# Kernel tuning notes

Measured on AMD Instinct MI355X. Metric: run time of the kernel, lower is better.

## Reference

```python
import jax, jax.numpy as jnp
import numpy as np

B, C, H, W = 4, 512, 64, 64
CK = C // 8  # key/query channels


def setup_inputs() -> dict:
    key = jax.random.key(0)
    ks = jax.random.split(key, 4)
    x = jax.random.normal(ks[0], (B, C, H, W), dtype=jnp.float32)
    # 1x1 conv weights -> plain [out, in] matrices; fan-in scaled like torch default-ish
    Wf = jax.random.normal(ks[1], (CK, C), dtype=jnp.float32) * (1.0 / np.sqrt(C))
    Wg = jax.random.normal(ks[2], (CK, C), dtype=jnp.float32) * (1.0 / np.sqrt(C))
    Wh = jax.random.normal(ks[3], (C, C), dtype=jnp.float32) * (1.0 / np.sqrt(C))
    bf = jnp.zeros((CK,), dtype=jnp.float32)
    bg = jnp.zeros((CK,), dtype=jnp.float32)
    bh = jnp.zeros((C,), dtype=jnp.float32)
    gamma = jnp.zeros((1,), dtype=jnp.float32)
    return {"x": x, "Wf": Wf, "bf": bf, "Wg": Wg, "bg": bg, "Wh": Wh, "bh": bh, "gamma": gamma}


def reference(x, Wf, bf, Wg, bg, Wh, bh, gamma):
    b, c, h, w = x.shape
    n = h * w
    xf = x.reshape(b, c, n)  # [B, C, N]
    # 1x1 convs == per-pixel linear maps
    f = jnp.einsum('kc,bcn->bkn', Wf, xf) + bf[None, :, None]  # [B, CK, N]
    g = jnp.einsum('kc,bcn->bkn', Wg, xf) + bg[None, :, None]  # [B, CK, N]
    hx = jnp.einsum('oc,bcn->bon', Wh, xf) + bh[None, :, None]  # [B, C, N]
    # energy[b,i,j] = sum_k f[b,k,i] * g[b,k,j]  (f_x.permute(0,2,1) @ g_x)
    energy = jnp.einsum('bki,bkj->bij', f, g)  # [B, N, N]
    attention = jax.nn.softmax(energy, axis=-1)
    # out[b,c,i] = sum_j hx[b,c,j] * attention[b,i,j]  (h_x @ attention^T)
    out = jnp.einsum('bcj,bij->bci', hx, attention)  # [B, C, N]
    out = out.reshape(b, c, h, w)
    return gamma[0] * out + x
```

## Files before the change

### kernel.cpp

```cpp
#include <hip/hip_runtime.h>
#include <hip/hip_bf16.h>

#define NB 4
#define CC 512
#define NN 4096
#define CKK 64

typedef _Float16 f16x8 __attribute__((ext_vector_type(8)));
typedef float    f32x4 __attribute__((ext_vector_type(4)));

__device__ __forceinline__ void g2l16(const _Float16* g, _Float16* l) {
    __builtin_amdgcn_global_load_lds(
        (const __attribute__((address_space(1))) void*)g,
        (__attribute__((address_space(3))) void*)l, 16, 0, 0);
}

__device__ __forceinline__ void stage_tile(const _Float16* __restrict__ g, int ldg,
                                           _Float16* lds, int lane, int wave) {
    #pragma unroll
    for (int r = 0; r < 2; r++) {
        int q = r * 4 + wave;
        int row = q * 16 + (lane >> 2);
        int col = (lane & 3) * 8;
        g2l16(g + (size_t)row * ldg + col, lds + q * 512 + lane * 8);
    }
}

__device__ __forceinline__ void stage_swz(const _Float16* __restrict__ g, int ldg,
                                          _Float16* lds, int tid) {
    int row = tid >> 2;
    int scq = (tid & 3) ^ ((row >> 1) & 3);
    g2l16(g + (size_t)row * ldg + scq * 8, lds + tid * 8);
}

__device__ __forceinline__ f16x8 rd_swz(const _Float16* lds, int row, int quad) {
    int q = quad ^ ((row >> 1) & 3);
    return *(const f16x8*)(lds + row * 32 + q * 8);
}

__launch_bounds__(256)
__global__ void prep(const float* __restrict__ x, _Float16* __restrict__ xT,
                     const float* __restrict__ Wf, const float* __restrict__ bf_,
                     const float* __restrict__ Wg, const float* __restrict__ bg_,
                     const float* __restrict__ Wh, const float* __restrict__ bh_,
                     _Float16* __restrict__ Wall, float* __restrict__ Ball) {
    const int N = NN, C = CC;
    int bid = blockIdx.x;
    int t = threadIdx.x;
    if (bid < 2048) {
        int n0 = (bid & 63) << 6;
        int c0 = ((bid >> 6) & 7) << 6;
        int b  = bid >> 9;
        __shared__ float T[64][65];
        const float* xb = x + (size_t)b * C * N;
        #pragma unroll
        for (int r = 0; r < 4; r++) {
            int c = (t >> 4) + 16 * r;
            int n4 = (t & 15) * 4;
            float4 v = *(const float4*)(xb + (size_t)(c0 + c) * N + n0 + n4);
            T[n4 + 0][c] = v.x; T[n4 + 1][c] = v.y; T[n4 + 2][c] = v.z; T[n4 + 3][c] = v.w;
        }
        __syncthreads();
        int n = t >> 2, cb = (t & 3) * 16;
        f16x8 h0, h1;
        #pragma unroll
        for (int i = 0; i < 8; i++) { h0[i] = (_Float16)T[n][cb + i]; h1[i] = (_Float16)T[n][cb + 8 + i]; }
        _Float16* dst = xT + (size_t)b * N * C + (size_t)(n0 + n) * C + c0 + cb;
        *(f16x8*)dst = h0;
        *(f16x8*)(dst + 8) = h1;
    } else {
        int o = bid - 2048;
        const float* src;
        if (o < 64)       src = Wf + (size_t)o * C;
        else if (o < 128) src = Wg + (size_t)(o - 64) * C;
        else              src = Wh + (size_t)(o - 128) * C;
        Wall[(size_t)o * C + t]       = (_Float16)src[t];
        Wall[(size_t)o * C + 256 + t] = (_Float16)src[256 + t];
        if (t == 0)
            Ball[o] = (o < 64) ? bf_[o] : (o < 128 ? bg_[o - 64] : bh_[o - 128]);
    }
}

__launch_bounds__(256)
__global__ void proj_mfma(const _Float16* __restrict__ xT, const _Float16* __restrict__ Wall,
                          const float* __restrict__ Ball,
                          _Float16* __restrict__ Ft, _Float16* __restrict__ Gt,
                          _Float16* __restrict__ Hx) {
    const int N = NN, C = CC;
    int n0 = blockIdx.x * 128;
    int o0 = blockIdx.y * 128;
    int b  = blockIdx.z;
    const _Float16* Arow = Wall + (size_t)o0 * C;
    const _Float16* Brow = xT + (size_t)b * N * C + (size_t)n0 * C;
    __shared__ _Float16 As[128 * 32];
    __shared__ _Float16 Bs[128 * 32];
    int tid = threadIdx.x, lane = tid & 63, wave = tid >> 6;
    int wm = wave & 1, wn = wave >> 1, lrow = lane & 15, quad = lane >> 4;
    f32x4 acc[4][4] = {};
    for (int kc = 0; kc < C; kc += 32) {
        __syncthreads();
        stage_tile(Arow + kc, C, As, lane, wave);
        stage_tile(Brow + kc, C, Bs, lane, wave);
        __syncthreads();
        f16x8 af[4], bf[4];
        #pragma unroll
        for (int mi = 0; mi < 4; mi++)
            af[mi] = *(const f16x8*)(As + (wm * 64 + mi * 16 + lrow) * 32 + quad * 8);
        #pragma unroll
        for (int ni = 0; ni < 4; ni++)
            bf[ni] = *(const f16x8*)(Bs + (wn * 64 + ni * 16 + lrow) * 32 + quad * 8);
        #pragma unroll
        for (int mi = 0; mi < 4; mi++)
            #pragma unroll
            for (int ni = 0; ni < 4; ni++)
                acc[mi][ni] = __builtin_amdgcn_mfma_f32_16x16x32_f16(af[mi], bf[ni], acc[mi][ni], 0, 0, 0);
    }
    float bias_r[4][4];
    #pragma unroll
    for (int mi = 0; mi < 4; mi++)
        #pragma unroll
        for (int r = 0; r < 4; r++)
            bias_r[mi][r] = Ball[o0 + wm * 64 + mi * 16 + quad * 4 + r];
    _Float16* Ftb = Ft + (size_t)b * NN * CKK;
    _Float16* Gtb = Gt + (size_t)b * NN * CKK;
    _Float16* Hxb = Hx + (size_t)b * CC * N;
    #pragma unroll
    for (int mi = 0; mi < 4; mi++)
        #pragma unroll
        for (int ni = 0; ni < 4; ni++)
            #pragma unroll
            for (int r = 0; r < 4; r++) {
                int o = o0 + wm * 64 + mi * 16 + quad * 4 + r;
                int n = n0 + wn * 64 + ni * 16 + lrow;
                _Float16 v = (_Float16)(acc[mi][ni][r] + bias_r[mi][r]);
                if (o < 64)       Ftb[(size_t)n * CKK + o] = v;
                else if (o < 128) Gtb[(size_t)n * CKK + (o - 64)] = v;
                else              Hxb[(size_t)(o - 128) * N + n] = v;
            }
}

#define PST_LD  136
#define MRED_LD 34
#define SM_FT    0
#define SM_BSG   16384
#define SM_PST   32768
#define SM_AH    67584
#define SM_MRED  100352
#define SM_MRUN  117760
#define SM_LRUN  118272
#define SM_OSC   118784
#define SM_TOTAL 119296

__launch_bounds__(512, 2)
__global__ void attn_fused(const _Float16* __restrict__ Ft, const _Float16* __restrict__ Gt,
                           const _Float16* __restrict__ Hx, const float* __restrict__ x,
                           const float* __restrict__ gamma, float* __restrict__ out) {
    const int N = NN, C = CC;
    extern __shared__ char smem[];
    _Float16* FtL = (_Float16*)(smem + SM_FT);
    _Float16* BsG = (_Float16*)(smem + SM_BSG);
    _Float16* Pst = (_Float16*)(smem + SM_PST);
    _Float16* Ah  = (_Float16*)(smem + SM_AH);
    float* Mred = (float*)(smem + SM_MRED);
    float* Mrun = (float*)(smem + SM_MRUN);
    float* Lrun = (float*)(smem + SM_LRUN);
    float* Osc  = (float*)(smem + SM_OSC);

    const int b  = blockIdx.z;
    const int i0 = blockIdx.x * 128;
    const int c0 = blockIdx.y * 256;
    const int tid = threadIdx.x;
    const int lane = tid & 63, w = tid >> 6;
    const int lrow = lane & 15, quad = lane >> 4;
    const int wi = w & 3, wj = w >> 2;
    const int wc = w >> 1, wi2 = w & 1;

    const _Float16* Ftb = Ft + (size_t)b * N * CKK + (size_t)i0 * CKK;
    const _Float16* Gtb = Gt + (size_t)b * N * CKK;
    const _Float16* Hxb = Hx + (size_t)b * C * N + (size_t)c0 * N;

    stage_swz(Ftb,      CKK, FtL,        tid);
    stage_swz(Ftb + 32, CKK, FtL + 4096, tid);
    if (tid < 128) { Mrun[tid] = -1e30f; Lrun[tid] = 0.0f; }
    __syncthreads();

    f16x8 afs[2][2];
    #pragma unroll
    for (int mi = 0; mi < 2; mi++)
        #pragma unroll
        for (int ks = 0; ks < 2; ks++)
            afs[mi][ks] = rd_swz(FtL + ks * 4096, wi * 32 + mi * 16 + lrow, quad);

    f32x4 acc[4][4] = {};

    for (int jt = 0; jt < NN / 128; jt++) {
        const _Float16* Gtr = Gtb + (size_t)jt * 128 * CKK;
        stage_swz(Gtr,      CKK, BsG,        tid);
        stage_swz(Gtr + 32, CKK, BsG + 4096, tid);
        __syncthreads();

        f32x4 sacc[2][4] = {};
        #pragma unroll
        for (int ks = 0; ks < 2; ks++)
            #pragma unroll
            for (int ni = 0; ni < 4; ni++) {
                f16x8 bfs = rd_swz(BsG + ks * 4096, wj * 64 + ni * 16 + lrow, quad);
                #pragma unroll
                for (int mi = 0; mi < 2; mi++)
                    sacc[mi][ni] = __builtin_amdgcn_mfma_f32_16x16x32_f16(afs[mi][ks], bfs, sacc[mi][ni], 0, 0, 0);
            }
        #pragma unroll
        for (int mi = 0; mi < 2; mi++)
            #pragma unroll
            for (int r = 0; r < 4; r++) {
                float v = fmaxf(fmaxf(sacc[mi][0][r], sacc[mi][1][r]),
                                fmaxf(sacc[mi][2][r], sacc[mi][3][r]));
                int row = wi * 32 + mi * 16 + quad * 4 + r;
                Mred[row * MRED_LD + wj * 16 + lrow] = v;
            }
        __syncthreads();
        if (tid < 128) {
            const float* mr = Mred + tid * MRED_LD;
            float mt = mr[0];
            #pragma unroll
            for (int k = 1; k < 32; k++) mt = fmaxf(mt, mr[k]);
            float mo = Mrun[tid];
            float mn = fmaxf(mo, mt);
            float sc = __expf(mo - mn);
            Mrun[tid] = mn;
            Osc[tid] = sc;
            Lrun[tid] *= sc;
        }
        __syncthreads();
        #pragma unroll
        for (int mi = 0; mi < 2; mi++)
            #pragma unroll
            for (int r = 0; r < 4; r++) {
                int row = wi * 32 + mi * 16 + quad * 4 + r;
                float m = Mrun[row];
                float ls = 0.f;
                #pragma unroll
                for (int ni = 0; ni < 4; ni++) {
                    float s16 = (float)(_Float16)sacc[mi][ni][r];
                    _Float16 p16 = (_Float16)__expf(s16 - m);
                    Pst[row * PST_LD + wj * 64 + ni * 16 + lrow] = p16;
                    ls += (float)p16;
                }
                Mred[row * MRED_LD + wj * 16 + lrow] = ls;
            }
        float scv[4];
        #pragma unroll
        for (int ni = 0; ni < 4; ni++) scv[ni] = Osc[wi2 * 64 + ni * 16 + lrow];
        #pragma unroll
        for (int mi = 0; mi < 4; mi++)
            #pragma unroll
            for (int ni = 0; ni < 4; ni++)
                #pragma unroll
                for (int r = 0; r < 4; r++)
                    acc[mi][ni][r] *= scv[ni];
        __syncthreads();
        if (tid < 128) {
            const float* mr = Mred + tid * MRED_LD;
            float s = 0.f;
            #pragma unroll
            for (int k = 0; k < 32; k++) s += mr[k];
            Lrun[tid] += s;
        }
        const _Float16* Hxr = Hxb + (size_t)jt * 128;
        stage_swz(Hxr,                   N, Ah,        tid);
        stage_swz(Hxr + (size_t)128 * N, N, Ah + 4096, tid);
        #pragma unroll
        for (int kk = 0; kk < 4; kk++) {
            if (kk < 3) {
                const _Float16* src = Hxr + (kk + 1) * 32;
                _Float16* dst = Ah + ((kk + 1) & 1) * 8192;
                stage_swz(src,                   N, dst,        tid);
                stage_swz(src + (size_t)128 * N, N, dst + 4096, tid);
            }
            __syncthreads();
            const _Float16* A = Ah + (kk & 1) * 8192;
            f16x8 bfv[4];
            #pragma unroll
            for (int ni = 0; ni < 4; ni++)
                bfv[ni] = *(const f16x8*)(Pst + (wi2 * 64 + ni * 16 + lrow) * PST_LD + kk * 32 + quad * 8);
            #pragma unroll
            for (int mi = 0; mi < 4; mi++) {
                f16x8 av = rd_swz(A, wc * 64 + mi * 16 + lrow, quad);
                #pragma unroll
                for (int ni = 0; ni < 4; ni++)
                    acc[mi][ni] = __builtin_amdgcn_mfma_f32_16x16x32_f16(av, bfv[ni], acc[mi][ni], 0, 0, 0);
            }
        }
    }
    __syncthreads();
    if (tid < 128) Osc[tid] = 1.0f / Lrun[tid];
    __syncthreads();
    float gv = gamma[0];
    const float* xb = x + (size_t)b * C * N;
    float* ob = out + (size_t)b * C * N;
    float li[4];
    #pragma unroll
    for (int ni = 0; ni < 4; ni++) li[ni] = Osc[wi2 * 64 + ni * 16 + lrow];
    #pragma unroll
    for (int mi = 0; mi < 4; mi++)
        #pragma unroll
        for (int ni = 0; ni < 4; ni++)
            #pragma unroll
            for (int r = 0; r < 4; r++) {
                int c = c0 + wc * 64 + mi * 16 + quad * 4 + r;
                int i = i0 + wi2 * 64 + ni * 16 + lrow;
                ob[(size_t)c * N + i] = gv * (acc[mi][ni][r] * li[ni]) + xb[(size_t)c * N + i];
            }
}

extern "C" void kernel_launch(void* const* d_in, const int* in_sizes, int n_in,
                              void* d_out, int out_size, void* d_ws, size_t ws_size,
                              hipStream_t stream) {
    const float* x     = (const float*)d_in[0];
    const float* Wf    = (const float*)d_in[1];
    const float* bf    = (const float*)d_in[2];
    const float* Wg    = (const float*)d_in[3];
    const float* bg    = (const float*)d_in[4];
    const float* Wh    = (const float*)d_in[5];
    const float* bh    = (const float*)d_in[6];
    const float* gamma = (const float*)d_in[7];
    float* out = (float*)d_out;

    char* wsb = (char*)d_ws;
    _Float16* Wall = (_Float16*)wsb;
    float*    Ball = (float*)(wsb + ((size_t)768 << 10));
    _Float16* Ft = (_Float16*)(wsb + ((size_t)1 << 20));
    _Float16* Gt = (_Float16*)(wsb + ((size_t)3 << 20));
    _Float16* Hx = (_Float16*)(wsb + ((size_t)5 << 20));
    _Float16* xT = (_Float16*)(wsb + ((size_t)21 << 20));

    prep<<<dim3(2048 + 640), dim3(256), 0, stream>>>(
        x, xT, Wf, bf, Wg, bg, Wh, bh, Wall, Ball);
    proj_mfma<<<dim3(NN / 128, 5, NB), dim3(256), 0, stream>>>(xT, Wall, Ball, Ft, Gt, Hx);

    hipFuncSetAttribute((const void*)attn_fused,
                        hipFuncAttributeMaxDynamicSharedMemorySize, SM_TOTAL);
    attn_fused<<<dim3(NN / 128, CC / 256, NB), dim3(512), SM_TOTAL, stream>>>(
        Ft, Gt, Hx, x, gamma, out);
}
```

Before: 275.3 us.

## Pipeline G and Hx tile loads with vmcnt barriers and shuffle-based softmax reductions

New measurement: 292.0 us. 6.1% more time.

```diff
diff --git a/kernel.cpp b/kernel.cpp
--- a/kernel.cpp
+++ b/kernel.cpp
@@ -5,9 +5,15 @@
 #define CC 512
 #define NN 4096
 #define CKK 64
-
+#define NT 32
+
+typedef _Float16 f16x4 __attribute__((ext_vector_type(4)));
 typedef _Float16 f16x8 __attribute__((ext_vector_type(8)));
 typedef float    f32x4 __attribute__((ext_vector_type(4)));
+
+#define BAR()       asm volatile("s_barrier" ::: "memory")
+#define BAR_LGKM()  asm volatile("s_waitcnt lgkmcnt(0)\n\ts_barrier" ::: "memory")
+#define BAR_VM(n)   asm volatile("s_waitcnt vmcnt(" #n ")\n\ts_barrier" ::: "memory")
 
 __device__ __forceinline__ void g2l16(const _Float16* g, _Float16* l) {
     __builtin_amdgcn_global_load_lds(
@@ -127,44 +133,50 @@
     #pragma unroll
     for (int mi = 0; mi < 4; mi++)
         #pragma unroll
-        for (int ni = 0; ni < 4; ni++)
-            #pragma unroll
-            for (int r = 0; r < 4; r++) {
-                int o = o0 + wm * 64 + mi * 16 + quad * 4 + r;
-                int n = n0 + wn * 64 + ni * 16 + lrow;
-                _Float16 v = (_Float16)(acc[mi][ni][r] + bias_r[mi][r]);
-                if (o < 64)       Ftb[(size_t)n * CKK + o] = v;
-                else if (o < 128) Gtb[(size_t)n * CKK + (o - 64)] = v;
-                else              Hxb[(size_t)(o - 128) * N + n] = v;
-            }
+        for (int ni = 0; ni < 4; ni++) {
+            int o = o0 + wm * 64 + mi * 16 + quad * 4;
+            int n = n0 + wn * 64 + ni * 16 + lrow;
+            f16x4 v;
+            #pragma unroll
+            for (int r = 0; r < 4; r++) v[r] = (_Float16)(acc[mi][ni][r] + bias_r[mi][r]);
+            if (o < 64)       *(f16x4*)(Ftb + (size_t)n * CKK + o) = v;
+            else if (o < 128) *(f16x4*)(Gtb + (size_t)n * CKK + (o - 64)) = v;
+            else {
+                #pragma unroll
+                for (int r = 0; r < 4; r++)
+                    Hxb[(size_t)(o - 128 + r) * N + n] = v[r];
+            }
+        }
 }
 
 #define PST_LD  136
-#define MRED_LD 34
+#define MRL     9
 #define SM_FT    0
 #define SM_BSG   16384
-#define SM_PST   32768
-#define SM_AH    67584
-#define SM_MRED  100352
-#define SM_MRUN  117760
-#define SM_LRUN  118272
-#define SM_OSC   118784
-#define SM_TOTAL 119296
+#define SM_PST   49152
+#define SM_AH    83968
+#define SM_MRED  149504
+#define SM_MRUN  154112
+#define SM_LRUN  154624
+#define SM_OSC   155136
+#define SM_FLAG  155648
+#define SM_TOTAL 155776
 
 __launch_bounds__(512, 2)
 __global__ void attn_fused(const _Float16* __restrict__ Ft, const _Float16* __restrict__ Gt,
                            const _Float16* __restrict__ Hx, const float* __restrict__ x,
                            const float* __restrict__ gamma, float* __restrict__ out) {
-    const int N = NN, C = CC;
+    const int N = NN;
     extern __shared__ char smem[];
-    _Float16* FtL = (_Float16*)(smem + SM_FT);
-    _Float16* BsG = (_Float16*)(smem + SM_BSG);
-    _Float16* Pst = (_Float16*)(smem + SM_PST);
-    _Float16* Ah  = (_Float16*)(smem + SM_AH);
+    _Float16* FtL  = (_Float16*)(smem + SM_FT);
+    _Float16* BsGp = (_Float16*)(smem + SM_BSG);
+    _Float16* Pst  = (_Float16*)(smem + SM_PST);
+    _Float16* AhL  = (_Float16*)(smem + SM_AH);
     float* Mred = (float*)(smem + SM_MRED);
     float* Mrun = (float*)(smem + SM_MRUN);
     float* Lrun = (float*)(smem + SM_LRUN);
     float* Osc  = (float*)(smem + SM_OSC);
+    int*   Fl   = (int*)(smem + SM_FLAG);
 
     const int b  = blockIdx.z;
     const int i0 = blockIdx.x * 128;
@@ -177,11 +189,14 @@
 
     const _Float16* Ftb = Ft + (size_t)b * N * CKK + (size_t)i0 * CKK;
     const _Float16* Gtb = Gt + (size_t)b * N * CKK;
-    const _Float16* Hxb = Hx + (size_t)b * C * N + (size_t)c0 * N;
+    const _Float16* Hxb = Hx + (size_t)b * CC * N + (size_t)c0 * N;
 
     stage_swz(Ftb,      CKK, FtL,        tid);
     stage_swz(Ftb + 32, CKK, FtL + 4096, tid);
+    stage_swz(Gtb,      CKK, BsGp,        tid);
+    stage_swz(Gtb + 32, CKK, BsGp + 4096, tid);
     if (tid < 128) { Mrun[tid] = -1e30f; Lrun[tid] = 0.0f; }
+    if (tid == 0) Fl[0] = 0;
     __syncthreads();
 
     f16x8 afs[2][2];
@@ -193,45 +208,74 @@
 
     f32x4 acc[4][4] = {};
 
-    for (int jt = 0; jt < NN / 128; jt++) {
-        const _Float16* Gtr = Gtb + (size_t)jt * 128 * CKK;
-        stage_swz(Gtr,      CKK, BsG,        tid);
-        stage_swz(Gtr + 32, CKK, BsG + 4096, tid);
-        __syncthreads();
-
+    #pragma unroll 1
+    for (int jt = 0; jt < NT; jt++) {
+        const int cur = jt & 1;
+        const _Float16* Hxr = Hxb + (size_t)jt * 128;
+        stage_swz(Hxr,                        N, AhL,         tid);
+        stage_swz(Hxr + (size_t)128 * N,      N, AhL + 4096,  tid);
+        stage_swz(Hxr + 32,                   N, AhL + 8192,  tid);
+        stage_swz(Hxr + 32 + (size_t)128 * N, N, AhL + 12288, tid);
+        stage_swz(Hxr + 64,                   N, AhL + 16384, tid);
+        stage_swz(Hxr + 64 + (size_t)128 * N, N, AhL + 20480, tid);
+        stage_swz(Hxr + 96,                   N, AhL + 24576, tid);
+        stage_swz(Hxr + 96 + (size_t)128 * N, N, AhL + 28672, tid);
+        const _Float16* Gn = Gtb + (size_t)((jt + 1) & (NT - 1)) * 128 * CKK;
+        _Float16* Gdst = BsGp + (cur ^ 1) * 8192;
+        stage_swz(Gn,      CKK, Gdst,        tid);
+        stage_swz(Gn + 32, CKK, Gdst + 4096, tid);
+        BAR_VM(10);
+
+        const _Float16* Bst = BsGp + cur * 8192;
         f32x4 sacc[2][4] = {};
         #pragma unroll
         for (int ks = 0; ks < 2; ks++)
             #pragma unroll
             for (int ni = 0; ni < 4; ni++) {
-                f16x8 bfs = rd_swz(BsG + ks * 4096, wj * 64 + ni * 16 + lrow, quad);
+                f16x8 bfs = rd_swz(Bst + ks * 4096, wj * 64 + ni * 16 + lrow, quad);
                 #pragma unroll
                 for (int mi = 0; mi < 2; mi++)
                     sacc[mi][ni] = __builtin_amdgcn_mfma_f32_16x16x32_f16(afs[mi][ks], bfs, sacc[mi][ni], 0, 0, 0);
             }
+        float red[8];
         #pragma unroll
         for (int mi = 0; mi < 2; mi++)
             #pragma unroll
-            for (int r = 0; r < 4; r++) {
-                float v = fmaxf(fmaxf(sacc[mi][0][r], sacc[mi][1][r]),
-                                fmaxf(sacc[mi][2][r], sacc[mi][3][r]));
-                int row = wi * 32 + mi * 16 + quad * 4 + r;
-                Mred[row * MRED_LD + wj * 16 + lrow] = v;
-            }
-        __syncthreads();
+            for (int r = 0; r < 4; r++)
+                red[mi * 4 + r] = fmaxf(fmaxf(sacc[mi][0][r], sacc[mi][1][r]),
+                                        fmaxf(sacc[mi][2][r], sacc[mi][3][r]));
+        #pragma unroll
+        for (int off = 1; off < 8; off <<= 1)
+            #pragma unroll
+            for (int s = 0; s < 8; s++)
+                red[s] = fmaxf(red[s], __shfl_xor(red[s], off));
+        if ((lrow & 7) == 0) {
+            #pragma unroll
+            for (int mi = 0; mi < 2; mi++)
+                #pragma unroll
+                for (int r = 0; r < 4; r++)
+                    Mred[(wi * 32 + mi * 16 + quad * 4 + r) * MRL + wj * 2 + (lrow >> 3)] = red[mi * 4 + r];
+        }
+        BAR_LGKM();
+
         if (tid < 128) {
-            const float* mr = Mred + tid * MRED_LD;
+            const float* mr = Mred + tid * MRL;
             float mt = mr[0];
             #pragma unroll
-            for (int k = 1; k < 32; k++) mt = fmaxf(mt, mr[k]);
+            for (int k = 1; k < 8; k++) mt = fmaxf(mt, mr[k]);
             float mo = Mrun[tid];
-            float mn = fmaxf(mo, mt);
-            float sc = __expf(mo - mn);
-            Mrun[tid] = mn;
-            Osc[tid] = sc;
-            Lrun[tid] *= sc;
-        }
-        __syncthreads();
+            if (mt > mo) {
+                Fl[0] = 1;
+                Mrun[tid] = mt;
+                float sc = __expf(mo - mt);
+                Osc[tid] = sc;
+                Lrun[tid] *= sc;
+            } else {
+                Osc[tid] = 1.0f;
+            }
+        }
+        BAR_LGKM();
+
         #pragma unroll
         for (int mi = 0; mi < 2; mi++)
             #pragma unroll
@@ -241,63 +285,77 @@
                 float ls = 0.f;
                 #pragma unroll
                 for (int ni = 0; ni < 4; ni++) {
-                    float s16 = (float)(_Float16)sacc[mi][ni][r];
-                    _Float16 p16 = (_Float16)__expf(s16 - m);
+                    _Float16 p16 = (_Float16)__expf(sacc[mi][ni][r] - m);
                     Pst[row * PST_LD + wj * 64 + ni * 16 + lrow] = p16;
                     ls += (float)p16;
                 }
-                Mred[row * MRED_LD + wj * 16 + lrow] = ls;
-            }
-        float scv[4];
-        #pragma unroll
-        for (int ni = 0; ni < 4; ni++) scv[ni] = Osc[wi2 * 64 + ni * 16 + lrow];
-        #pragma unroll
-        for (int mi = 0; mi < 4; mi++)
-            #pragma unroll
-            for (int ni = 0; ni < 4; ni++)
+                red[mi * 4 + r] = ls;
+            }
+        #pragma unroll
+        for (int off = 1; off < 8; off <<= 1)
+            #pragma unroll
+            for (int s = 0; s < 8; s++)
+                red[s] += __shfl_xor(red[s], off);
+        if ((lrow & 7) == 0) {
+            #pragma unroll
+            for (int mi = 0; mi < 2; mi++)
                 #pragma unroll
                 for (int r = 0; r < 4; r++)
-                    acc[mi][ni][r] *= scv[ni];
-        __syncthreads();
+                    Mred[(wi * 32 + mi * 16 + quad * 4 + r) * MRL + wj * 2 + (lrow >> 3)] = red[mi * 4 + r];
+        }
+        if (Fl[0]) {
+            float scv[4];
+            #pragma unroll
+            for (int ni = 0; ni < 4; ni++) scv[ni] = Osc[wi2 * 64 + ni * 16 + lrow];
+            #pragma unroll
+            for (int mi = 0; mi < 4; mi++)
+                #pragma unroll
+                for (int ni = 0; ni < 4; ni++)
+                    #pragma unroll
+                    for (int r = 0; r < 4; r++)
+                        acc[mi][ni][r] *= scv[ni];
+        }
+        BAR_LGKM();
+
         if (tid < 128) {
-            const float* mr = Mred + tid * MRED_LD;
+            const float* mr = Mred + tid * MRL;
             float s = 0.f;
             #pragma unroll
-            for (int k = 0; k < 32; k++) s += mr[k];
+            for (int k = 0; k < 8; k++) s += mr[k];
             Lrun[tid] += s;
         }
-        const _Float16* Hxr = Hxb + (size_t)jt * 128;
-        stage_swz(Hxr,                   N, Ah,        tid);
-        stage_swz(Hxr + (size_t)128 * N, N, Ah + 4096, tid);
-        #pragma unroll
-        for (int kk = 0; kk < 4; kk++) {
-            if (kk < 3) {
-                const _Float16* src = Hxr + (kk + 1) * 32;
-                _Float16* dst = Ah + ((kk + 1) & 1) * 8192;
-                stage_swz(src,                   N, dst,        tid);
-                stage_swz(src + (size_t)128 * N, N, dst + 4096, tid);
-            }
-            __syncthreads();
-            const _Float16* A = Ah + (kk & 1) * 8192;
-            f16x8 bfv[4];
-            #pragma unroll
-            for (int ni = 0; ni < 4; ni++)
-                bfv[ni] = *(const f16x8*)(Pst + (wi2 * 64 + ni * 16 + lrow) * PST_LD + kk * 32 + quad * 8);
-            #pragma unroll
-            for (int mi = 0; mi < 4; mi++) {
-                f16x8 av = rd_swz(A, wc * 64 + mi * 16 + lrow, quad);
+        if (tid == 0) Fl[0] = 0;
+
+        auto pv_half = [&](const _Float16* Ab, int kb) {
+            #pragma unroll
+            for (int ks2 = 0; ks2 < 2; ks2++) {
+                f16x8 bfv[4];
                 #pragma unroll
                 for (int ni = 0; ni < 4; ni++)
-                    acc[mi][ni] = __builtin_amdgcn_mfma_f32_16x16x32_f16(av, bfv[ni], acc[mi][ni], 0, 0, 0);
-            }
-        }
+                    bfv[ni] = *(const f16x8*)(Pst + (wi2 * 64 + ni * 16 + lrow) * PST_LD + (kb + ks2) * 32 + quad * 8);
+                #pragma unroll
+                for (int mi = 0; mi < 4; mi++) {
+                    f16x8 av = rd_swz(Ab + ks2 * 8192, wc * 64 + mi * 16 + lrow, quad);
+                    #pragma unroll
+                    for (int ni = 0; ni < 4; ni++)
+                        acc[mi][ni] = __builtin_amdgcn_mfma_f32_16x16x32_f16(av, bfv[ni], acc[mi][ni], 0, 0, 0);
+                }
+            }
+        };
+        BAR_VM(6);
+        pv_half(AhL, 0);
+        BAR_VM(2);
+        pv_half(AhL + 16384, 2);
+        BAR();
     }
+
     __syncthreads();
     if (tid < 128) Osc[tid] = 1.0f / Lrun[tid];
     __syncthreads();
+
     float gv = gamma[0];
-    const float* xb = x + (size_t)b * C * N;
-    float* ob = out + (size_t)b * C * N;
+    const float* xb = x + (size_t)b * CC * N;
+    float* ob = out + (size_t)b * CC * N;
     float li[4];
     #pragma unroll
     for (int ni = 0; ni < 4; ni++) li[ni] = Osc[wi2 * 64 + ni * 16 + lrow];
@@ -334,12 +392,16 @@
     _Float16* Hx = (_Float16*)(wsb + ((size_t)5 << 20));
     _Float16* xT = (_Float16*)(wsb + ((size_t)21 << 20));
 
+    static const bool attn_attr_once = [] {
+        hipFuncSetAttribute((const void*)attn_fused,
+                            hipFuncAttributeMaxDynamicSharedMemorySize, SM_TOTAL);
+        return true;
+    }();
+    (void)attn_attr_once;
+
     prep<<<dim3(2048 + 640), dim3(256), 0, stream>>>(
         x, xT, Wf, bf, Wg, bg, Wh, bh, Wall, Ball);
     proj_mfma<<<dim3(NN / 128, 5, NB), dim3(256), 0, stream>>>(xT, Wall, Ball, Ft, Gt, Hx);
-
-    hipFuncSetAttribute((const void*)attn_fused,
-                        hipFuncAttributeMaxDynamicSharedMemorySize, SM_TOTAL);
     attn_fused<<<dim3(NN / 128, CC / 256, NB), dim3(512), SM_TOTAL, stream>>>(
         Ft, Gt, Hx, x, gamma, out);
 }
```

## Restructure attention kernel to per-wave softmax with register P and shuffles

Applied to the files above, without the earlier changes.

New measurement: 416.5 us. 1.51x slower.

```diff
diff --git a/kernel.cpp b/kernel.cpp
--- a/kernel.cpp
+++ b/kernel.cpp
@@ -5,7 +5,9 @@
 #define CC 512
 #define NN 4096
 #define CKK 64
-
+#define NT 32
+
+typedef _Float16 f16x4 __attribute__((ext_vector_type(4)));
 typedef _Float16 f16x8 __attribute__((ext_vector_type(8)));
 typedef float    f32x4 __attribute__((ext_vector_type(4)));
 
@@ -36,6 +38,12 @@
 __device__ __forceinline__ f16x8 rd_swz(const _Float16* lds, int row, int quad) {
     int q = quad ^ ((row >> 1) & 3);
     return *(const f16x8*)(lds + row * 32 + q * 8);
+}
+
+__device__ __forceinline__ uint32_t pkh(float a, float b) {
+    union { _Float16 h[2]; uint32_t u; } v;
+    v.h[0] = (_Float16)a; v.h[1] = (_Float16)b;
+    return v.u;
 }
 
 __launch_bounds__(256)
@@ -127,190 +135,156 @@
     #pragma unroll
     for (int mi = 0; mi < 4; mi++)
         #pragma unroll
-        for (int ni = 0; ni < 4; ni++)
-            #pragma unroll
-            for (int r = 0; r < 4; r++) {
-                int o = o0 + wm * 64 + mi * 16 + quad * 4 + r;
-                int n = n0 + wn * 64 + ni * 16 + lrow;
-                _Float16 v = (_Float16)(acc[mi][ni][r] + bias_r[mi][r]);
-                if (o < 64)       Ftb[(size_t)n * CKK + o] = v;
-                else if (o < 128) Gtb[(size_t)n * CKK + (o - 64)] = v;
-                else              Hxb[(size_t)(o - 128) * N + n] = v;
+        for (int ni = 0; ni < 4; ni++) {
+            int o = o0 + wm * 64 + mi * 16 + quad * 4;
+            int n = n0 + wn * 64 + ni * 16 + lrow;
+            f16x4 v;
+            #pragma unroll
+            for (int r = 0; r < 4; r++) v[r] = (_Float16)(acc[mi][ni][r] + bias_r[mi][r]);
+            if (o < 64)       *(f16x4*)(Ftb + (size_t)n * CKK + o) = v;
+            else if (o < 128) *(f16x4*)(Gtb + (size_t)n * CKK + (o - 64)) = v;
+            else {
+                #pragma unroll
+                for (int r = 0; r < 4; r++)
+                    Hxb[(size_t)(o - 128 + r) * N + n] = v[r];
             }
-}
-
-#define PST_LD  136
-#define MRED_LD 34
-#define SM_FT    0
-#define SM_BSG   16384
-#define SM_PST   32768
-#define SM_AH    67584
-#define SM_MRED  100352
-#define SM_MRUN  117760
-#define SM_LRUN  118272
-#define SM_OSC   118784
-#define SM_TOTAL 119296
-
-__launch_bounds__(512, 2)
+        }
+}
+
+#define SM_TOTAL 65536
+
+__launch_bounds__(512, 4)
 __global__ void attn_fused(const _Float16* __restrict__ Ft, const _Float16* __restrict__ Gt,
                            const _Float16* __restrict__ Hx, const float* __restrict__ x,
                            const float* __restrict__ gamma, float* __restrict__ out) {
-    const int N = NN, C = CC;
+    const int N = NN;
     extern __shared__ char smem[];
-    _Float16* FtL = (_Float16*)(smem + SM_FT);
-    _Float16* BsG = (_Float16*)(smem + SM_BSG);
-    _Float16* Pst = (_Float16*)(smem + SM_PST);
-    _Float16* Ah  = (_Float16*)(smem + SM_AH);
-    float* Mred = (float*)(smem + SM_MRED);
-    float* Mrun = (float*)(smem + SM_MRUN);
-    float* Lrun = (float*)(smem + SM_LRUN);
-    float* Osc  = (float*)(smem + SM_OSC);
-
-    const int b  = blockIdx.z;
-    const int i0 = blockIdx.x * 128;
-    const int c0 = blockIdx.y * 256;
+    _Float16* AhL = (_Float16*)smem;
+
+    int h = blockIdx.x;
+    int l = (h & 7) * 64 + (h >> 3);
+    int bx = l & 31;
+    int rem = l >> 5;
+    int by = rem & 3;
+    int b  = rem >> 2;
+    const int i0 = bx * 128;
+    const int c0 = by * 128;
+
     const int tid = threadIdx.x;
     const int lane = tid & 63, w = tid >> 6;
     const int lrow = lane & 15, quad = lane >> 4;
-    const int wi = w & 3, wj = w >> 2;
-    const int wc = w >> 1, wi2 = w & 1;
-
-    const _Float16* Ftb = Ft + (size_t)b * N * CKK + (size_t)i0 * CKK;
+
+    const _Float16* Ftb = Ft + ((size_t)b * N + i0 + w * 16) * CKK;
     const _Float16* Gtb = Gt + (size_t)b * N * CKK;
-    const _Float16* Hxb = Hx + (size_t)b * C * N + (size_t)c0 * N;
-
-    stage_swz(Ftb,      CKK, FtL,        tid);
-    stage_swz(Ftb + 32, CKK, FtL + 4096, tid);
-    if (tid < 128) { Mrun[tid] = -1e30f; Lrun[tid] = 0.0f; }
-    __syncthreads();
-
-    f16x8 afs[2][2];
-    #pragma unroll
-    for (int mi = 0; mi < 2; mi++)
+    const _Float16* Hxb = Hx + ((size_t)b * CC + c0) * N;
+
+    #pragma unroll
+    for (int kk = 0; kk < 4; kk++)
+        stage_swz(Hxb + kk * 32, N, AhL + kk * 4096, tid);
+
+    f16x8 ftf[2];
+    #pragma unroll
+    for (int ks = 0; ks < 2; ks++)
+        ftf[ks] = *(const f16x8*)(Ftb + (size_t)lrow * CKK + ks * 32 + quad * 8);
+
+    f32x4 acc[8] = {};
+    float m_run = -1e30f, l_run = 0.0f;
+    const int src0 = (quad & 1) * 32 + lrow;
+    const int src1 = src0 + 16;
+
+    #pragma unroll 1
+    for (int jt = 0; jt < NT; jt++) {
+        const int p = jt & 1;
+        {
+            const int jn = (jt + 1) & (NT - 1);
+            const _Float16* Hn = Hxb + (size_t)jn * 128;
+            _Float16* dst = AhL + (p ^ 1) * 16384;
+            #pragma unroll
+            for (int kk = 0; kk < 4; kk++)
+                stage_swz(Hn + kk * 32, N, dst + kk * 4096, tid);
+        }
+        f32x4 sacc[8] = {};
+        const _Float16* Gr = Gtb + (size_t)jt * 128 * CKK;
         #pragma unroll
         for (int ks = 0; ks < 2; ks++)
-            afs[mi][ks] = rd_swz(FtL + ks * 4096, wi * 32 + mi * 16 + lrow, quad);
-
-    f32x4 acc[4][4] = {};
-
-    for (int jt = 0; jt < NN / 128; jt++) {
-        const _Float16* Gtr = Gtb + (size_t)jt * 128 * CKK;
-        stage_swz(Gtr,      CKK, BsG,        tid);
-        stage_swz(Gtr + 32, CKK, BsG + 4096, tid);
-        __syncthreads();
-
-        f32x4 sacc[2][4] = {};
-        #pragma unroll
-        for (int ks = 0; ks < 2; ks++)
-            #pragma unroll
-            for (int ni = 0; ni < 4; ni++) {
-                f16x8 bfs = rd_swz(BsG + ks * 4096, wj * 64 + ni * 16 + lrow, quad);
-                #pragma unroll
-                for (int mi = 0; mi < 2; mi++)
-                    sacc[mi][ni] = __builtin_amdgcn_mfma_f32_16x16x32_f16(afs[mi][ks], bfs, sacc[mi][ni], 0, 0, 0);
+            #pragma unroll
+            for (int jf = 0; jf < 8; jf++) {
+                f16x8 ga = *(const f16x8*)(Gr + (size_t)(jf * 16 + lrow) * CKK + ks * 32 + quad * 8);
+                sacc[jf] = __builtin_amdgcn_mfma_f32_16x16x32_f16(ga, ftf[ks], sacc[jf], 0, 0, 0);
             }
-        #pragma unroll
-        for (int mi = 0; mi < 2; mi++)
-            #pragma unroll
-            for (int r = 0; r < 4; r++) {
-                float v = fmaxf(fmaxf(sacc[mi][0][r], sacc[mi][1][r]),
-                                fmaxf(sacc[mi][2][r], sacc[mi][3][r]));
-                int row = wi * 32 + mi * 16 + quad * 4 + r;
-                Mred[row * MRED_LD + wj * 16 + lrow] = v;
+        float mt;
+        {
+            float m0 = fmaxf(fmaxf(sacc[0][0], sacc[0][1]), fmaxf(sacc[0][2], sacc[0][3]));
+            #pragma unroll
+            for (int jf = 1; jf < 8; jf++) {
+                float mv = fmaxf(fmaxf(sacc[jf][0], sacc[jf][1]), fmaxf(sacc[jf][2], sacc[jf][3]));
+                m0 = fmaxf(m0, mv);
             }
-        __syncthreads();
-        if (tid < 128) {
-            const float* mr = Mred + tid * MRED_LD;
-            float mt = mr[0];
-            #pragma unroll
-            for (int k = 1; k < 32; k++) mt = fmaxf(mt, mr[k]);
-            float mo = Mrun[tid];
-            float mn = fmaxf(mo, mt);
-            float sc = __expf(mo - mn);
-            Mrun[tid] = mn;
-            Osc[tid] = sc;
-            Lrun[tid] *= sc;
-        }
-        __syncthreads();
-        #pragma unroll
-        for (int mi = 0; mi < 2; mi++)
-            #pragma unroll
-            for (int r = 0; r < 4; r++) {
-                int row = wi * 32 + mi * 16 + quad * 4 + r;
-                float m = Mrun[row];
-                float ls = 0.f;
-                #pragma unroll
-                for (int ni = 0; ni < 4; ni++) {
-                    float s16 = (float)(_Float16)sacc[mi][ni][r];
-                    _Float16 p16 = (_Float16)__expf(s16 - m);
-                    Pst[row * PST_LD + wj * 64 + ni * 16 + lrow] = p16;
-                    ls += (float)p16;
-                }
-                Mred[row * MRED_LD + wj * 16 + lrow] = ls;
+            m0 = fmaxf(m0, __shfl_xor(m0, 16));
+            mt = fmaxf(m0, __shfl_xor(m0, 32));
+        }
+        const float mn = fmaxf(m_run, mt);
+        const float sc = __expf(m_run - mn);
+        m_run = mn;
+        #pragma unroll
+        for (int cf = 0; cf < 8; cf++)
+            #pragma unroll
+            for (int r = 0; r < 4; r++)
+                acc[cf][r] *= sc;
+        uint32_t p01[8], p23[8];
+        float ls = 0.0f;
+        #pragma unroll
+        for (int jf = 0; jf < 8; jf++) {
+            float e0 = __expf(sacc[jf][0] - mn);
+            float e1 = __expf(sacc[jf][1] - mn);
+            float e2 = __expf(sacc[jf][2] - mn);
+            float e3 = __expf(sacc[jf][3] - mn);
+            ls += (e0 + e1) + (e2 + e3);
+            p01[jf] = pkh(e0, e1);
+            p23[jf] = pkh(e2, e3);
+        }
+        ls += __shfl_xor(ls, 16);
+        ls += __shfl_xor(ls, 32);
+        l_run = l_run * sc + ls;
+        asm volatile("s_waitcnt vmcnt(4)\n\ts_barrier" ::: "memory");
+        const _Float16* Ab = AhL + p * 16384;
+        #pragma unroll
+        for (int kk = 0; kk < 4; kk++) {
+            uint32_t a0 = __shfl(p01[2 * kk], src0);
+            uint32_t a1 = __shfl(p23[2 * kk], src0);
+            uint32_t a2 = __shfl(p01[2 * kk], src1);
+            uint32_t a3 = __shfl(p23[2 * kk], src1);
+            uint32_t b0 = __shfl(p01[2 * kk + 1], src0);
+            uint32_t b1 = __shfl(p23[2 * kk + 1], src0);
+            uint32_t b2 = __shfl(p01[2 * kk + 1], src1);
+            uint32_t b3 = __shfl(p23[2 * kk + 1], src1);
+            union { uint32_t u[4]; f16x8 v; } bb;
+            bool hi = (quad & 2) != 0;
+            bb.u[0] = hi ? b0 : a0;
+            bb.u[1] = hi ? b1 : a1;
+            bb.u[2] = hi ? b2 : a2;
+            bb.u[3] = hi ? b3 : a3;
+            #pragma unroll
+            for (int cf = 0; cf < 8; cf++) {
+                f16x8 av = rd_swz(Ab + kk * 4096, cf * 16 + lrow, quad);
+                acc[cf] = __builtin_amdgcn_mfma_f32_16x16x32_f16(av, bb.v, acc[cf], 0, 0, 0);
             }
-        float scv[4];
-        #pragma unroll
-        for (int ni = 0; ni < 4; ni++) scv[ni] = Osc[wi2 * 64 + ni * 16 + lrow];
-        #pragma unroll
-        for (int mi = 0; mi < 4; mi++)
-            #pragma unroll
-            for (int ni = 0; ni < 4; ni++)
-                #pragma unroll
-                for (int r = 0; r < 4; r++)
-                    acc[mi][ni][r] *= scv[ni];
-        __syncthreads();
-        if (tid < 128) {
-            const float* mr = Mred + tid * MRED_LD;
-            float s = 0.f;
-            #pragma unroll
-            for (int k = 0; k < 32; k++) s += mr[k];
-            Lrun[tid] += s;
-        }
-        const _Float16* Hxr = Hxb + (size_t)jt * 128;
-        stage_swz(Hxr,                   N, Ah,        tid);
-        stage_swz(Hxr + (size_t)128 * N, N, Ah + 4096, tid);
-        #pragma unroll
-        for (int kk = 0; kk < 4; kk++) {
-            if (kk < 3) {
-                const _Float16* src = Hxr + (kk + 1) * 32;
-                _Float16* dst = Ah + ((kk + 1) & 1) * 8192;
-                stage_swz(src,                   N, dst,        tid);
-                stage_swz(src + (size_t)128 * N, N, dst + 4096, tid);
-            }
-            __syncthreads();
-            const _Float16* A = Ah + (kk & 1) * 8192;
-            f16x8 bfv[4];
-            #pragma unroll
-            for (int ni = 0; ni < 4; ni++)
-                bfv[ni] = *(const f16x8*)(Pst + (wi2 * 64 + ni * 16 + lrow) * PST_LD + kk * 32 + quad * 8);
-            #pragma unroll
-            for (int mi = 0; mi < 4; mi++) {
-                f16x8 av = rd_swz(A, wc * 64 + mi * 16 + lrow, quad);
-                #pragma unroll
-                for (int ni = 0; ni < 4; ni++)
-                    acc[mi][ni] = __builtin_amdgcn_mfma_f32_16x16x32_f16(av, bfv[ni], acc[mi][ni], 0, 0, 0);
-            }
-        }
+        }
+        asm volatile("s_barrier" ::: "memory");
     }
-    __syncthreads();
-    if (tid < 128) Osc[tid] = 1.0f / Lrun[tid];
-    __syncthreads();
-    float gv = gamma[0];
-    const float* xb = x + (size_t)b * C * N;
-    float* ob = out + (size_t)b * C * N;
-    float li[4];
-    #pragma unroll
-    for (int ni = 0; ni < 4; ni++) li[ni] = Osc[wi2 * 64 + ni * 16 + lrow];
-    #pragma unroll
-    for (int mi = 0; mi < 4; mi++)
-        #pragma unroll
-        for (int ni = 0; ni < 4; ni++)
-            #pragma unroll
-            for (int r = 0; r < 4; r++) {
-                int c = c0 + wc * 64 + mi * 16 + quad * 4 + r;
-                int i = i0 + wi2 * 64 + ni * 16 + lrow;
-                ob[(size_t)c * N + i] = gv * (acc[mi][ni][r] * li[ni]) + xb[(size_t)c * N + i];
-            }
+
+    const float gv = gamma[0];
+    const float li = 1.0f / l_run;
+    const float* xb = x + (size_t)b * CC * N;
+    float* ob = out + (size_t)b * CC * N;
+    const int iG = i0 + w * 16 + lrow;
+    #pragma unroll
+    for (int cf = 0; cf < 8; cf++)
+        #pragma unroll
+        for (int r = 0; r < 4; r++) {
+            int c = c0 + cf * 16 + quad * 4 + r;
+            ob[(size_t)c * N + iG] = gv * (acc[cf][r] * li) + xb[(size_t)c * N + iG];
+        }
 }
 
 extern "C" void kernel_launch(void* const* d_in, const int* in_sizes, int n_in,
@@ -334,12 +308,16 @@
     _Float16* Hx = (_Float16*)(wsb + ((size_t)5 << 20));
     _Float16* xT = (_Float16*)(wsb + ((size_t)21 << 20));
 
+    static const bool attn_attr_once = [] {
+        hipFuncSetAttribute((const void*)attn_fused,
+                            hipFuncAttributeMaxDynamicSharedMemorySize, SM_TOTAL);
+        return true;
+    }();
+    (void)attn_attr_once;
+
     prep<<<dim3(2048 + 640), dim3(256), 0, stream>>>(
         x, xT, Wf, bf, Wg, bg, Wh, bh, Wall, Ball);
     proj_mfma<<<dim3(NN / 128, 5, NB), dim3(256), 0, stream>>>(xT, Wall, Ball, Ft, Gt, Hx);
-
-    hipFuncSetAttribute((const void*)attn_fused,
-                        hipFuncAttributeMaxDynamicSharedMemorySize, SM_TOTAL);
-    attn_fused<<<dim3(NN / 128, CC / 256, NB), dim3(512), SM_TOTAL, stream>>>(
+    attn_fused<<<dim3(512), dim3(512), SM_TOTAL, stream>>>(
         Ft, Gt, Hx, x, gamma, out);
 }
```
